# Kernel tuning notes

Measured on AMD Instinct MI355X. Metric: run time of the kernel, lower is better.

The kernel has to match this reference:

```python
import jax, jax.numpy as jnp
import numpy as np

B, Z, H, T = 4096, 512, 384, 32


def setup_inputs() -> dict:
    key = jax.random.key(0)
    ks = jax.random.split(key, 8)
    z = jax.random.normal(ks[0], (B, Z), dtype=jnp.float32)
    h_init = jax.random.normal(ks[1], (B, H), dtype=jnp.float32) * 0.01
    s1 = 1.0 / np.sqrt(Z)
    s23 = 1.0 / np.sqrt(2 * H)
    W1 = jax.random.uniform(ks[2], (H, Z), jnp.float32, -s1, s1)
    b1 = jax.random.uniform(ks[3], (H,), jnp.float32, -s1, s1)
    W2 = jax.random.uniform(ks[4], (Z, 2 * H), jnp.float32, -s23, s23)
    b2 = jax.random.uniform(ks[5], (Z,), jnp.float32, -s23, s23)
    W3 = jax.random.uniform(ks[6], (H, 2 * H), jnp.float32, -s23, s23)
    b3 = jax.random.uniform(ks[7], (H,), jnp.float32, -s23, s23)
    return {"z": z, "h_init": h_init, "W1": W1, "b1": b1, "W2": W2,
            "b2": b2, "W3": W3, "b3": b3, "n_frames": T}


def reference(z, h_init, W1, b1, W2, b2, W3, b3, n_frames):
    # training path: r = w_residual*4 / n_frames (const decay)
    r = jnp.asarray(0.2 * 4.0 / n_frames, dtype=z.dtype)
    lrelu = lambda x: jax.nn.leaky_relu(x, 0.01)

    def step(carry, _):
        zp, hp = carry
        temp = jnp.concatenate([lrelu(zp @ W1.T + b1), hp], axis=-1)  # [B, 2H]
        zn = lrelu(temp @ W2.T + b2) * r + zp
        hn = lrelu(temp @ W3.T + b3) * r + hp
        return (zn, hn), zn

    _, outs = jax.lax.scan(step, (z, h_init), None, length=n_frames - 1)
    all_out = jnp.concatenate([z[None], outs], axis=0)        # [T, B, Z]
    out = (all_out - z[None]).transpose(1, 0, 2)               # [B, T, Z]
    return out.reshape(-1, z.shape[-1])                        # [B*T, Z]
```

## Files before the change

kernel.cpp:

```cpp
#include <hip/hip_runtime.h>
#include <type_traits>


typedef _Float16 f16;
typedef f16 f16x8 __attribute__((ext_vector_type(8)));
typedef float f32x4 __attribute__((ext_vector_type(4)));
typedef float f32x16 __attribute__((ext_vector_type(16)));

#define ZD 512
#define HD 384
#define TT 32
#define BM 32
#define LZ 516
#define LT 392

__device__ __forceinline__ float lrelu(float x) { return x >= 0.f ? x : 0.01f * x; }

__global__ void cvt_f32_f16(const float* __restrict__ s, f16* __restrict__ d, int n) {
    for (int i = blockIdx.x * blockDim.x + threadIdx.x; i < n; i += gridDim.x * blockDim.x)
        d[i] = (f16)s[i];
}

__global__ __launch_bounds__(512) void latrec(
    const float* __restrict__ z0g, const float* __restrict__ h0g,
    const f16* __restrict__ W1h, const f16* __restrict__ W2h, const f16* __restrict__ W3h,
    const float* __restrict__ b1g, const float* __restrict__ b2g, const float* __restrict__ b3g,
    float* __restrict__ out)
{
    __shared__ float zf[BM * LZ];
    __shared__ f16 tz[BM * LT];
    __shared__ f16 hb[2][BM * LT];
    __shared__ float bias[1280];

    const int tid = threadIdx.x;
    const int w = tid >> 6, l = tid & 63;
    const int lm = l & 31;
    const int lk = (l >> 5) * 8;
    const int m0 = blockIdx.x * BM;

    for (int i = tid; i < HD; i += 512) bias[i] = b1g[i];
    for (int i = tid; i < ZD; i += 512) bias[384 + i] = b2g[i];
    for (int i = tid; i < HD; i += 512) bias[896 + i] = b3g[i];
    for (int i = tid; i < BM * 128; i += 512) {
        int r = i >> 7, c = (i & 127) << 2;
        f32x4 v = *(const f32x4*)(z0g + (size_t)(m0 + r) * ZD + c);
        *(f32x4*)(zf + r * LZ + c) = v;
        f32x4 zr = {0.f, 0.f, 0.f, 0.f};
        __builtin_nontemporal_store(zr.x, out + ((size_t)(m0 + r) * TT) * ZD + c);
        __builtin_nontemporal_store(zr.y, out + ((size_t)(m0 + r) * TT) * ZD + c + 1);
        __builtin_nontemporal_store(zr.z, out + ((size_t)(m0 + r) * TT) * ZD + c + 2);
        __builtin_nontemporal_store(zr.w, out + ((size_t)(m0 + r) * TT) * ZD + c + 3);
    }
    for (int i = tid; i < BM * HD; i += 512) {
        int r = i / HD, c = i - r * HD;
        hb[0][r * LT + c] = (f16)h0g[(size_t)(m0 + r) * HD + c];
    }
    __syncthreads();

    for (int t = 1; t < TT; ++t) {
        const f16* hcur = hb[(t - 1) & 1];
        f16* hnxt = hb[t & 1];

        {
            const int nt0 = (w < 4) ? 2 * w : (w + 4);
            const int nt1 = (w < 4) ? 2 * w + 1 : nt0;
            const float* ap = zf + lm * LZ + lk;
            const f16* wp0 = W1h + (size_t)(nt0 * 32 + lm) * ZD + lk;
            const f16* wp1 = W1h + (size_t)(nt1 * 32 + lm) * ZD + lk;
            auto run1 = [&](auto NTC) {
                constexpr int NT = decltype(NTC)::value;
                f32x16 a0 = {}, a1 = {};
                #pragma unroll 4
                for (int ks = 0; ks < ZD; ks += 16) {
                    f32x4 x0 = *(const f32x4*)(ap + ks);
                    f32x4 x1 = *(const f32x4*)(ap + ks + 4);
                    f16x8 af;
                    #pragma unroll
                    for (int e = 0; e < 4; ++e) { af[e] = (f16)x0[e]; af[4 + e] = (f16)x1[e]; }
                    f16x8 bf0 = *(const f16x8*)(wp0 + ks);
                    a0 = __builtin_amdgcn_mfma_f32_32x32x16_f16(af, bf0, a0, 0, 0, 0);
                    if constexpr (NT == 2) {
                        f16x8 bf1 = *(const f16x8*)(wp1 + ks);
                        a1 = __builtin_amdgcn_mfma_f32_32x32x16_f16(af, bf1, a1, 0, 0, 0);
                    }
                }
                {
                    int c = nt0 * 32 + lm; float bv = bias[c];
                    #pragma unroll
                    for (int rg = 0; rg < 16; ++rg) {
                        int row = (rg & 3) + 8 * (rg >> 2) + 4 * (l >> 5);
                        tz[row * LT + c] = (f16)lrelu(a0[rg] + bv);
                    }
                }
                if constexpr (NT == 2) {
                    int c = nt1 * 32 + lm; float bv = bias[c];
                    #pragma unroll
                    for (int rg = 0; rg < 16; ++rg) {
                        int row = (rg & 3) + 8 * (rg >> 2) + 4 * (l >> 5);
                        tz[row * LT + c] = (f16)lrelu(a1[rg] + bv);
                    }
                }
            };
            if (w < 4) run1(std::integral_constant<int, 2>{});
            else       run1(std::integral_constant<int, 1>{});
        }
        __syncthreads();

        {
            const int t0 = w, t1 = w + 8;
            const int t2 = (w < 4) ? 16 + 2 * w : 20 + w;
            const int t3 = (w < 4) ? 17 + 2 * w : t2;
            auto wptr = [&](int nt) {
                return (nt < 16) ? W2h + (size_t)(nt * 32 + lm) * 768 + lk
                                 : W3h + (size_t)((nt - 16) * 32 + lm) * 768 + lk;
            };
            const f16* wp0 = wptr(t0); const f16* wp1 = wptr(t1);
            const f16* wp2 = wptr(t2); const f16* wp3 = wptr(t3);
            const f16* ap1 = tz + lm * LT + lk;
            const f16* ap2 = hcur + lm * LT + lk;

            auto epi2 = [&](const f32x16& ac, int nt) {
                if (nt < 16) {
                    int c = nt * 32 + lm;
                    float bv = bias[384 + c];
                    #pragma unroll
                    for (int rg = 0; rg < 16; ++rg) {
                        int row = (rg & 3) + 8 * (rg >> 2) + 4 * (l >> 5);
                        float v = lrelu(ac[rg] + bv) * 0.025f;
                        float zn = zf[row * LZ + c] + v;
                        zf[row * LZ + c] = zn;
                        size_t gr = (size_t)(m0 + row);
                        float o = zn - z0g[gr * ZD + c];
                        __builtin_nontemporal_store(o, out + (gr * TT + t) * ZD + c);
                    }
                } else {
                    int c = (nt - 16) * 32 + lm;
                    float bv = bias[896 + c];
                    #pragma unroll
                    for (int rg = 0; rg < 16; ++rg) {
                        int row = (rg & 3) + 8 * (rg >> 2) + 4 * (l >> 5);
                        float v = lrelu(ac[rg] + bv) * 0.025f;
                        float hn = (float)hcur[row * LT + c] + v;
                        hnxt[row * LT + c] = (f16)hn;
                    }
                }
            };

            auto run2 = [&](auto NTC) {
                constexpr int NT = decltype(NTC)::value;
                f32x16 a0 = {}, a1 = {}, a2 = {}, a3 = {};
                auto khalf = [&](const f16* ab, int kw) {
                    #pragma unroll 4
                    for (int ks = 0; ks < HD; ks += 16) {
                        f16x8 af = *(const f16x8*)(ab + ks);
                        f16x8 b0 = *(const f16x8*)(wp0 + kw + ks);
                        a0 = __builtin_amdgcn_mfma_f32_32x32x16_f16(af, b0, a0, 0, 0, 0);
                        f16x8 b1 = *(const f16x8*)(wp1 + kw + ks);
                        a1 = __builtin_amdgcn_mfma_f32_32x32x16_f16(af, b1, a1, 0, 0, 0);
                        f16x8 b2 = *(const f16x8*)(wp2 + kw + ks);
                        a2 = __builtin_amdgcn_mfma_f32_32x32x16_f16(af, b2, a2, 0, 0, 0);
                        if constexpr (NT == 4) {
                            f16x8 b3 = *(const f16x8*)(wp3 + kw + ks);
                            a3 = __builtin_amdgcn_mfma_f32_32x32x16_f16(af, b3, a3, 0, 0, 0);
                        }
                    }
                };
                khalf(ap1, 0);
                khalf(ap2, HD);
                epi2(a0, t0); epi2(a1, t1); epi2(a2, t2);
                if constexpr (NT == 4) epi2(a3, t3);
            };
            if (w < 4) run2(std::integral_constant<int, 4>{});
            else       run2(std::integral_constant<int, 3>{});
        }
        __syncthreads();
    }
}

extern "C" void kernel_launch(void* const* d_in, const int* in_sizes, int n_in,
                              void* d_out, int out_size, void* d_ws, size_t ws_size,
                              hipStream_t stream) {
    const float* z  = (const float*)d_in[0];
    const float* h0 = (const float*)d_in[1];
    const float* W1 = (const float*)d_in[2];
    const float* b1 = (const float*)d_in[3];
    const float* W2 = (const float*)d_in[4];
    const float* b2 = (const float*)d_in[5];
    const float* W3 = (const float*)d_in[6];
    const float* b3 = (const float*)d_in[7];
    float* out = (float*)d_out;

    char* p = (char*)d_ws;
    f16* W1h = (f16*)p; p += (size_t)HD * ZD * 2;
    f16* W2h = (f16*)p; p += (size_t)ZD * 768 * 2;
    f16* W3h = (f16*)p; p += (size_t)HD * 768 * 2;

    cvt_f32_f16<<<96, 256, 0, stream>>>(W1, W1h, HD * ZD);
    cvt_f32_f16<<<192, 256, 0, stream>>>(W2, W2h, ZD * 768);
    cvt_f32_f16<<<144, 256, 0, stream>>>(W3, W3h, HD * 768);

    latrec<<<4096 / BM, 512, 0, stream>>>(z, h0, W1h, W2h, W3h, b1, b2, b3, out);
}
```

Measured before the change: 1.843 ms.

## Pre-swizzle weights into MFMA fragment order and use 1024-thread blocks with register z state

Weights are rearranged on the device into MFMA-fragment order so each lane reads contiguous 16-byte chunks, and the weight loads are software-pipelined three k-steps ahead. The block grows to 16 waves, so each wave owns one output tile per GEMM. The z state moves from an fp32 shared array into accumulator registers, with only an fp16 copy kept in shared memory, and h is updated in place inside the concatenated temp buffer. The aim is better latency hiding and coalesced weight fetches; the cost is more register pressure, an extra barrier per step, and fp16 rounding of the z fed to the first GEMM.

```diff
diff --git a/kernel.cpp b/kernel.cpp
--- a/kernel.cpp
+++ b/kernel.cpp
@@ -4,174 +4,161 @@
 
 typedef _Float16 f16;
 typedef f16 f16x8 __attribute__((ext_vector_type(8)));
-typedef float f32x4 __attribute__((ext_vector_type(4)));
 typedef float f32x16 __attribute__((ext_vector_type(16)));
 
 #define ZD 512
 #define HD 384
 #define TT 32
 #define BM 32
-#define LZ 516
-#define LT 392
+#define LZH 520
+#define LTP 776
 
 __device__ __forceinline__ float lrelu(float x) { return x >= 0.f ? x : 0.01f * x; }
 
-__global__ void cvt_f32_f16(const float* __restrict__ s, f16* __restrict__ d, int n) {
-    for (int i = blockIdx.x * blockDim.x + threadIdx.x; i < n; i += gridDim.x * blockDim.x)
-        d[i] = (f16)s[i];
+__global__ void swz(const float* __restrict__ W, f16* __restrict__ dst, int N, int K) {
+    int nk = K >> 4;
+    int total = (N >> 5) * nk * 64;
+    for (int f = blockIdx.x * blockDim.x + threadIdx.x; f < total; f += gridDim.x * blockDim.x) {
+        int l = f & 63, c = f >> 6;
+        int ks = c % nk, nt = c / nk;
+        const float* s = W + (size_t)(nt * 32 + (l & 31)) * K + ks * 16 + (l >> 5) * 8;
+        f16* d = dst + (size_t)f * 8;
+        #pragma unroll
+        for (int e = 0; e < 8; ++e) d[e] = (f16)s[e];
+    }
 }
 
-__global__ __launch_bounds__(512) void latrec(
+__global__ __launch_bounds__(1024, 4) void latrec(
     const float* __restrict__ z0g, const float* __restrict__ h0g,
-    const f16* __restrict__ W1h, const f16* __restrict__ W2h, const f16* __restrict__ W3h,
+    const f16* __restrict__ W1s, const f16* __restrict__ W23s,
     const float* __restrict__ b1g, const float* __restrict__ b2g, const float* __restrict__ b3g,
     float* __restrict__ out)
 {
-    __shared__ float zf[BM * LZ];
-    __shared__ f16 tz[BM * LT];
-    __shared__ f16 hb[2][BM * LT];
+    __shared__ f16 zh[BM * LZH];
+    __shared__ f16 tp[BM * LTP];
     __shared__ float bias[1280];
 
     const int tid = threadIdx.x;
     const int w = tid >> 6, l = tid & 63;
-    const int lm = l & 31;
-    const int lk = (l >> 5) * 8;
+    const int lm = l & 31, lk8 = (l >> 5) * 8;
     const int m0 = blockIdx.x * BM;
 
-    for (int i = tid; i < HD; i += 512) bias[i] = b1g[i];
-    for (int i = tid; i < ZD; i += 512) bias[384 + i] = b2g[i];
-    for (int i = tid; i < HD; i += 512) bias[896 + i] = b3g[i];
-    for (int i = tid; i < BM * 128; i += 512) {
-        int r = i >> 7, c = (i & 127) << 2;
-        f32x4 v = *(const f32x4*)(z0g + (size_t)(m0 + r) * ZD + c);
-        *(f32x4*)(zf + r * LZ + c) = v;
-        f32x4 zr = {0.f, 0.f, 0.f, 0.f};
-        __builtin_nontemporal_store(zr.x, out + ((size_t)(m0 + r) * TT) * ZD + c);
-        __builtin_nontemporal_store(zr.y, out + ((size_t)(m0 + r) * TT) * ZD + c + 1);
-        __builtin_nontemporal_store(zr.z, out + ((size_t)(m0 + r) * TT) * ZD + c + 2);
-        __builtin_nontemporal_store(zr.w, out + ((size_t)(m0 + r) * TT) * ZD + c + 3);
+    for (int i = tid; i < HD; i += 1024) bias[i] = b1g[i];
+    for (int i = tid; i < ZD; i += 1024) bias[HD + i] = b2g[i];
+    for (int i = tid; i < HD; i += 1024) bias[896 + i] = b3g[i];
+    for (int i = tid; i < BM * ZD; i += 1024) {
+        int r = i >> 9, c = i & 511;
+        float v = z0g[(size_t)(m0 + r) * ZD + c];
+        zh[r * LZH + c] = (f16)v;
+        out[((size_t)(m0 + r) * TT) * ZD + c] = 0.f;
     }
-    for (int i = tid; i < BM * HD; i += 512) {
+    for (int i = tid; i < BM * HD; i += 1024) {
         int r = i / HD, c = i - r * HD;
-        hb[0][r * LT + c] = (f16)h0g[(size_t)(m0 + r) * HD + c];
+        tp[r * LTP + HD + c] = (f16)h0g[(size_t)(m0 + r) * HD + c];
+    }
+    f32x16 zm;
+    {
+        int c = w * 32 + lm;
+        #pragma unroll
+        for (int rg = 0; rg < 16; ++rg) {
+            int row = (rg & 3) + 8 * (rg >> 2) + 4 * (l >> 5);
+            zm[rg] = z0g[(size_t)(m0 + row) * ZD + c];
+        }
     }
     __syncthreads();
 
+    const bool hash = (w < 4) || (w >= 8);
+    const int ht = (w < 4) ? w : (w - 4);
+    const f16* zbs = W23s + (size_t)w * 24576 + (size_t)l * 8;
+    const f16* hbs = W23s + (size_t)(16 + ht) * 24576 + (size_t)l * 8;
+    const float rr = 0.025f;
+
     for (int t = 1; t < TT; ++t) {
-        const f16* hcur = hb[(t - 1) & 1];
-        f16* hnxt = hb[t & 1];
-
-        {
-            const int nt0 = (w < 4) ? 2 * w : (w + 4);
-            const int nt1 = (w < 4) ? 2 * w + 1 : nt0;
-            const float* ap = zf + lm * LZ + lk;
-            const f16* wp0 = W1h + (size_t)(nt0 * 32 + lm) * ZD + lk;
-            const f16* wp1 = W1h + (size_t)(nt1 * 32 + lm) * ZD + lk;
-            auto run1 = [&](auto NTC) {
-                constexpr int NT = decltype(NTC)::value;
-                f32x16 a0 = {}, a1 = {};
-                #pragma unroll 4
-                for (int ks = 0; ks < ZD; ks += 16) {
-                    f32x4 x0 = *(const f32x4*)(ap + ks);
-                    f32x4 x1 = *(const f32x4*)(ap + ks + 4);
-                    f16x8 af;
-                    #pragma unroll
-                    for (int e = 0; e < 4; ++e) { af[e] = (f16)x0[e]; af[4 + e] = (f16)x1[e]; }
-                    f16x8 bf0 = *(const f16x8*)(wp0 + ks);
-                    a0 = __builtin_amdgcn_mfma_f32_32x32x16_f16(af, bf0, a0, 0, 0, 0);
-                    if constexpr (NT == 2) {
-                        f16x8 bf1 = *(const f16x8*)(wp1 + ks);
-                        a1 = __builtin_amdgcn_mfma_f32_32x32x16_f16(af, bf1, a1, 0, 0, 0);
-                    }
-                }
-                {
-                    int c = nt0 * 32 + lm; float bv = bias[c];
-                    #pragma unroll
-                    for (int rg = 0; rg < 16; ++rg) {
-                        int row = (rg & 3) + 8 * (rg >> 2) + 4 * (l >> 5);
-                        tz[row * LT + c] = (f16)lrelu(a0[rg] + bv);
-                    }
-                }
-                if constexpr (NT == 2) {
-                    int c = nt1 * 32 + lm; float bv = bias[c];
-                    #pragma unroll
-                    for (int rg = 0; rg < 16; ++rg) {
-                        int row = (rg & 3) + 8 * (rg >> 2) + 4 * (l >> 5);
-                        tz[row * LT + c] = (f16)lrelu(a1[rg] + bv);
-                    }
-                }
-            };
-            if (w < 4) run1(std::integral_constant<int, 2>{});
-            else       run1(std::integral_constant<int, 1>{});
+        if (w < 12) {
+            const f16* bs = W1s + (size_t)w * 16384 + (size_t)l * 8;
+            const f16* ap = zh + lm * LZH + lk8;
+            f32x16 acc = {};
+            f16x8 b0 = *(const f16x8*)(bs);
+            f16x8 b1 = *(const f16x8*)(bs + 512);
+            f16x8 b2 = *(const f16x8*)(bs + 1024);
+            #pragma unroll
+            for (int ks = 0; ks < 32; ++ks) {
+                f16x8 a = *(const f16x8*)(ap + ks * 16);
+                f16x8 bn{};
+                if (ks + 3 < 32) bn = *(const f16x8*)(bs + (size_t)(ks + 3) * 512);
+                acc = __builtin_amdgcn_mfma_f32_32x32x16_f16(a, b0, acc, 0, 0, 0);
+                b0 = b1; b1 = b2; b2 = bn;
+            }
+            int c = w * 32 + lm;
+            float bv = bias[c];
+            #pragma unroll
+            for (int rg = 0; rg < 16; ++rg) {
+                int row = (rg & 3) + 8 * (rg >> 2) + 4 * (l >> 5);
+                tp[row * LTP + c] = (f16)lrelu(acc[rg] + bv);
+            }
         }
         __syncthreads();
 
+        f32x16 az = {}, ah = {};
         {
-            const int t0 = w, t1 = w + 8;
-            const int t2 = (w < 4) ? 16 + 2 * w : 20 + w;
-            const int t3 = (w < 4) ? 17 + 2 * w : t2;
-            auto wptr = [&](int nt) {
-                return (nt < 16) ? W2h + (size_t)(nt * 32 + lm) * 768 + lk
-                                 : W3h + (size_t)((nt - 16) * 32 + lm) * 768 + lk;
-            };
-            const f16* wp0 = wptr(t0); const f16* wp1 = wptr(t1);
-            const f16* wp2 = wptr(t2); const f16* wp3 = wptr(t3);
-            const f16* ap1 = tz + lm * LT + lk;
-            const f16* ap2 = hcur + lm * LT + lk;
-
-            auto epi2 = [&](const f32x16& ac, int nt) {
-                if (nt < 16) {
-                    int c = nt * 32 + lm;
-                    float bv = bias[384 + c];
-                    #pragma unroll
-                    for (int rg = 0; rg < 16; ++rg) {
-                        int row = (rg & 3) + 8 * (rg >> 2) + 4 * (l >> 5);
-                        float v = lrelu(ac[rg] + bv) * 0.025f;
-                        float zn = zf[row * LZ + c] + v;
-                        zf[row * LZ + c] = zn;
-                        size_t gr = (size_t)(m0 + row);
-                        float o = zn - z0g[gr * ZD + c];
-                        __builtin_nontemporal_store(o, out + (gr * TT + t) * ZD + c);
+            const f16* ap = tp + lm * LTP + lk8;
+            auto kloop = [&](auto HASH) {
+                f16x8 z0r = *(const f16x8*)(zbs);
+                f16x8 z1r = *(const f16x8*)(zbs + 512);
+                f16x8 z2r = *(const f16x8*)(zbs + 1024);
+                f16x8 h0r{}, h1r{}, h2r{};
+                if constexpr (decltype(HASH)::value) {
+                    h0r = *(const f16x8*)(hbs);
+                    h1r = *(const f16x8*)(hbs + 512);
+                    h2r = *(const f16x8*)(hbs + 1024);
+                }
+                #pragma unroll
+                for (int ks = 0; ks < 48; ++ks) {
+                    f16x8 a = *(const f16x8*)(ap + ks * 16);
+                    f16x8 zn{}, hn{};
+                    if (ks + 3 < 48) {
+                        zn = *(const f16x8*)(zbs + (size_t)(ks + 3) * 512);
+                        if constexpr (decltype(HASH)::value)
+                            hn = *(const f16x8*)(hbs + (size_t)(ks + 3) * 512);
                     }
-                } else {
-                    int c = (nt - 16) * 32 + lm;
-                    float bv = bias[896 + c];
-                    #pragma unroll
-                    for (int rg = 0; rg < 16; ++rg) {
-                        int row = (rg & 3) + 8 * (rg >> 2) + 4 * (l >> 5);
-                        float v = lrelu(ac[rg] + bv) * 0.025f;
-                        float hn = (float)hcur[row * LT + c] + v;
-                        hnxt[row * LT + c] = (f16)hn;
-                    }
+                    az = __builtin_amdgcn_mfma_f32_32x32x16_f16(a, z0r, az, 0, 0, 0);
+                    if constexpr (decltype(HASH)::value)
+                        ah = __builtin_amdgcn_mfma_f32_32x32x16_f16(a, h0r, ah, 0, 0, 0);
+                    z0r = z1r; z1r = z2r; z2r = zn;
+                    if constexpr (decltype(HASH)::value) { h0r = h1r; h1r = h2r; h2r = hn; }
                 }
             };
+            if (hash) kloop(std::true_type{});
+            else      kloop(std::false_type{});
+        }
 
-            auto run2 = [&](auto NTC) {
-                constexpr int NT = decltype(NTC)::value;
-                f32x16 a0 = {}, a1 = {}, a2 = {}, a3 = {};
-                auto khalf = [&](const f16* ab, int kw) {
-                    #pragma unroll 4
-                    for (int ks = 0; ks < HD; ks += 16) {
-                        f16x8 af = *(const f16x8*)(ab + ks);
-                        f16x8 b0 = *(const f16x8*)(wp0 + kw + ks);
-                        a0 = __builtin_amdgcn_mfma_f32_32x32x16_f16(af, b0, a0, 0, 0, 0);
-                        f16x8 b1 = *(const f16x8*)(wp1 + kw + ks);
-                        a1 = __builtin_amdgcn_mfma_f32_32x32x16_f16(af, b1, a1, 0, 0, 0);
-                        f16x8 b2 = *(const f16x8*)(wp2 + kw + ks);
-                        a2 = __builtin_amdgcn_mfma_f32_32x32x16_f16(af, b2, a2, 0, 0, 0);
-                        if constexpr (NT == 4) {
-                            f16x8 b3 = *(const f16x8*)(wp3 + kw + ks);
-                            a3 = __builtin_amdgcn_mfma_f32_32x32x16_f16(af, b3, a3, 0, 0, 0);
-                        }
-                    }
-                };
-                khalf(ap1, 0);
-                khalf(ap2, HD);
-                epi2(a0, t0); epi2(a1, t1); epi2(a2, t2);
-                if constexpr (NT == 4) epi2(a3, t3);
-            };
-            if (w < 4) run2(std::integral_constant<int, 4>{});
-            else       run2(std::integral_constant<int, 3>{});
+        {
+            int c = w * 32 + lm;
+            float bv = bias[HD + c];
+            #pragma unroll
+            for (int rg = 0; rg < 16; ++rg) {
+                int row = (rg & 3) + 8 * (rg >> 2) + 4 * (l >> 5);
+                float v = lrelu(az[rg] + bv) * rr;
+                float zn2 = zm[rg] + v;
+                zm[rg] = zn2;
+                zh[row * LZH + c] = (f16)zn2;
+                size_t gr = (size_t)(m0 + row);
+                float o = zn2 - z0g[gr * ZD + c];
+                __builtin_nontemporal_store(o, out + (gr * TT + t) * ZD + c);
+            }
+        }
+        __syncthreads();
+        if (hash) {
+            int c2 = ht * 32 + lm;
+            float bv = bias[896 + c2];
+            #pragma unroll
+            for (int rg = 0; rg < 16; ++rg) {
+                int row = (rg & 3) + 8 * (rg >> 2) + 4 * (l >> 5);
+                float v = lrelu(ah[rg] + bv) * rr;
+                int a = row * LTP + HD + c2;
+                float hn2 = (float)tp[a] + v;
+                tp[a] = (f16)hn2;
+            }
         }
         __syncthreads();
     }
@@ -191,13 +178,12 @@
     float* out = (float*)d_out;
 
     char* p = (char*)d_ws;
-    f16* W1h = (f16*)p; p += (size_t)HD * ZD * 2;
-    f16* W2h = (f16*)p; p += (size_t)ZD * 768 * 2;
-    f16* W3h = (f16*)p; p += (size_t)HD * 768 * 2;
+    f16* W1s  = (f16*)p; p += (size_t)HD * ZD * 2;
+    f16* W23s = (f16*)p; p += (size_t)(ZD + HD) * 768 * 2;
 
-    cvt_f32_f16<<<96, 256, 0, stream>>>(W1, W1h, HD * ZD);
-    cvt_f32_f16<<<192, 256, 0, stream>>>(W2, W2h, ZD * 768);
-    cvt_f32_f16<<<144, 256, 0, stream>>>(W3, W3h, HD * 768);
+    swz<<<96, 256, 0, stream>>>(W1, W1s, HD, ZD);
+    swz<<<192, 256, 0, stream>>>(W2, W23s, ZD, 768);
+    swz<<<144, 256, 0, stream>>>(W3, W23s + (size_t)16 * 24576, HD, 768);
 
-    latrec<<<4096 / BM, 512, 0, stream>>>(z, h0, W1h, W2h, W3h, b1, b2, b3, out);
+    latrec<<<4096 / BM, 1024, 0, stream>>>(z, h0, W1s, W23s, b1, b2, b3, out);
 }
```

Result: slower. 2.023 ms (+9.8%).
